# Kernel tuning notes

Hardware: AMD Instinct MI355X
Metric: run time of the kernel (lower is better)

## Reference

```python
import jax, jax.numpy as jnp
import numpy as np

N_ATOMS = 100000
IN_F = 512
HID = 512
OUT_F = 256
N_SPECIES = 64
EMB_DIM = 16
N_ROUTED = 6
N_SHARED = 2
TOPK = 2


def setup_inputs() -> dict:
    key = jax.random.key(0)
    ks = jax.random.split(key, 12)
    s = 0.02
    return {
        "features": jax.random.normal(ks[0], (N_ATOMS, IN_F), dtype=jnp.float32),
        "species_idx": jax.random.randint(ks[1], (N_ATOMS,), 0, N_SPECIES),
        "emb": jax.random.normal(ks[2], (N_SPECIES, EMB_DIM), dtype=jnp.float32),
        "W_router": jax.random.normal(ks[3], (N_ROUTED, EMB_DIM), dtype=jnp.float32) * s,
        "rW1": jax.random.normal(ks[4], (N_ROUTED, HID, IN_F), dtype=jnp.float32) * s,
        "rb1": jax.random.normal(ks[5], (N_ROUTED, HID), dtype=jnp.float32) * s,
        "rW2": jax.random.normal(ks[6], (N_ROUTED, OUT_F, HID), dtype=jnp.float32) * s,
        "rb2": jax.random.normal(ks[7], (N_ROUTED, OUT_F), dtype=jnp.float32) * s,
        "sW1": jax.random.normal(ks[8], (N_SHARED, HID, IN_F), dtype=jnp.float32) * s,
        "sb1": jax.random.normal(ks[9], (N_SHARED, HID), dtype=jnp.float32) * s,
        "sW2": jax.random.normal(ks[10], (N_SHARED, OUT_F, HID), dtype=jnp.float32) * s,
        "sb2": jax.random.normal(ks[11], (N_SHARED, OUT_F), dtype=jnp.float32) * s,
    }


def _expert_mlp(x, W1, b1, W2, b2):
    # x: [n, d]; W1: [E, h, d]; W2: [E, o, h] -> [n, E, o]
    h = jax.nn.silu(jnp.einsum("nd,ehd->neh", x, W1) + b1)
    return jnp.einsum("neh,eoh->neo", h, W2) + b2


def reference(features, species_idx, emb, W_router, rW1, rb1, rW2, rb2, sW1, sb1, sW2, sb2):
    # Router: u = SiLU(Embedding(z)); scores = softmax(W_e u)
    u = jax.nn.silu(emb[species_idx])                    # [n, M]
    scores = jax.nn.softmax(u @ W_router.T, axis=-1)     # [n, I]
    topk_scores, topk_idx = jax.lax.top_k(scores, TOPK)
    n = scores.shape[0]
    routing_weights = jnp.zeros_like(scores).at[
        jnp.arange(n)[:, None], topk_idx
    ].set(topk_scores)                                   # sparse gates [n, I]

    routed = _expert_mlp(features, rW1, rb1, rW2, rb2)   # [n, I, o]
    out = jnp.einsum("ne,neo->no", routing_weights, routed)

    shared = _expert_mlp(features, sW1, sb1, sW2, sb2)   # [n, S, o]
    return out + shared.sum(axis=1)
```

## Files before the change

kernel.cpp:

```cpp
#include <hip/hip_runtime.h>
#include <hip/hip_bf16.h>


typedef __attribute__((ext_vector_type(8))) short short8;
typedef __attribute__((ext_vector_type(4))) float f32x4;

#define IN_F 512
#define HID  512
#define OUT_F 256
#define TILE 64
#define CH   8192

#define WAIT_LGKM0 asm volatile("s_waitcnt lgkmcnt(0)" ::: "memory")
#define WAIT_VM2   asm volatile("s_waitcnt vmcnt(2)"   ::: "memory")
#define WAIT_VM0   asm volatile("s_waitcnt vmcnt(0)"   ::: "memory")

__device__ inline unsigned short f2bf(float f) {
    __hip_bfloat16 h = __float2bfloat16(f);
    return *reinterpret_cast<unsigned short*>(&h);
}

__device__ __forceinline__ void dma16(const unsigned short* g, unsigned short* l) {
    __builtin_amdgcn_global_load_lds(
        (const __attribute__((address_space(1))) unsigned int*)(unsigned long long)(const void*)g,
        (__attribute__((address_space(3))) unsigned int*)(unsigned int)(unsigned long long)(void*)l,
        16, 0, 0);
}

__device__ __forceinline__ void stage_chunk(const unsigned short* g,
                                            unsigned short* l, int w, int lane) {
    dma16(g + w * 1024 +       lane * 8, l + w * 1024);
    dma16(g + w * 1024 + 512 + lane * 8, l + w * 1024 + 512);
}

__global__ void k_cvt_w1(const float* __restrict__ rW1, const float* __restrict__ sW1,
                         unsigned short* __restrict__ dst) {
    int i = blockIdx.x * 256 + threadIdx.x;
    int low3 = i & 7;
    int sw   = (i >> 3) & 3;
    int row  = (i >> 5) & 255;
    int kq   = (i >> 13) & 15;
    int j    = (i >> 17) & 1;
    int ex   = i >> 18;
    int col  = ((sw ^ ((row >> 1) & 3)) << 3) + low3;
    int hrow = j * 256 + row;
    int kcol = kq * 32 + col;
    float v = (ex < 6) ? rW1[((size_t)ex * 512 + hrow) * 512 + kcol]
                       : sW1[((size_t)(ex - 6) * 512 + hrow) * 512 + kcol];
    dst[i] = f2bf(v);
}

__global__ void k_cvt_w2(const float* __restrict__ rW2, const float* __restrict__ sW2,
                         unsigned short* __restrict__ dst) {
    int i = blockIdx.x * 256 + threadIdx.x;
    int low3 = i & 7;
    int sw   = (i >> 3) & 3;
    int row  = (i >> 5) & 255;
    int kq   = (i >> 13) & 7;
    int j    = (i >> 16) & 1;
    int ex   = i >> 17;
    int col  = ((sw ^ ((row >> 1) & 3)) << 3) + low3;
    int kcol = j * 256 + kq * 32 + col;
    float v = (ex < 6) ? rW2[((size_t)ex * 256 + row) * 512 + kcol]
                       : sW2[((size_t)(ex - 6) * 256 + row) * 512 + kcol];
    dst[i] = f2bf(v);
}

__global__ void k_fill(int* __restrict__ counts, int* __restrict__ cursors,
                       int* __restrict__ idxl, int* __restrict__ tile_pair,
                       int CAP, int TMAX) {
    int i = blockIdx.x * 256 + threadIdx.x;
    if (i < 16) { counts[i] = 0; cursors[i] = 0; }
    if (i < TMAX) tile_pair[i] = -1;
    if (i < CAP) idxl[i] = -1;
}

__global__ void k_router(const int* __restrict__ species, const float* __restrict__ emb,
                         const float* __restrict__ Wr,
                         int* __restrict__ pid, float* __restrict__ gA, float* __restrict__ gB,
                         int* __restrict__ counts, int N) {
    __shared__ int lcnt[16];
    int tid = threadIdx.x;
    if (tid < 16) lcnt[tid] = 0;
    __syncthreads();
    int i = blockIdx.x * 256 + tid;
    if (i < N) {
        int z = species[i];
        float u[16];
#pragma unroll
        for (int k = 0; k < 16; ++k) {
            float v = emb[z * 16 + k];
            u[k] = v / (1.f + __expf(-v));
        }
        float s[6];
        float mx = -1e30f;
#pragma unroll
        for (int e = 0; e < 6; ++e) {
            float a = 0.f;
#pragma unroll
            for (int k = 0; k < 16; ++k) a += u[k] * Wr[e * 16 + k];
            s[e] = a;
            mx = fmaxf(mx, a);
        }
        float sum = 0.f;
#pragma unroll
        for (int e = 0; e < 6; ++e) { s[e] = __expf(s[e] - mx); sum += s[e]; }
        float inv = 1.f / sum;
        int i0 = 0;
#pragma unroll
        for (int e = 1; e < 6; ++e) if (s[e] > s[i0]) i0 = e;
        int i1 = (i0 == 0) ? 1 : 0;
#pragma unroll
        for (int e = 0; e < 6; ++e) if (e != i0 && s[e] > s[i1]) i1 = e;
        float g0 = s[i0] * inv, g1 = s[i1] * inv;
        int a = min(i0, i1), b = max(i0, i1);
        const int PB[5] = {0, 5, 9, 12, 14};
        int p = PB[a] + (b - a - 1);
        pid[i] = p;
        gA[i] = (a == i0) ? g0 : g1;
        gB[i] = (a == i0) ? g1 : g0;
        atomicAdd(&lcnt[p], 1);
    }
    __syncthreads();
    if (tid < 15 && lcnt[tid] > 0) atomicAdd(&counts[tid], lcnt[tid]);
}

__global__ void k_scan(const int* __restrict__ counts, int* __restrict__ offs,
                       int* __restrict__ tile_pair, int TMAX) {
    __shared__ int so[16];
    if (threadIdx.x == 0) {
        int acc = 0;
        for (int p = 0; p < 15; ++p) { so[p] = acc; acc += (counts[p] + 63) & ~63; }
        so[15] = acc;
        for (int p = 0; p < 16; ++p) offs[p] = so[p];
    }
    __syncthreads();
    for (int t = threadIdx.x; t < TMAX; t += blockDim.x) {
        int t64 = t * 64;
        if (t64 < so[15]) {
            int p = 0;
            while (!(t64 >= so[p] && t64 < so[p + 1])) ++p;
            tile_pair[t] = p;
        }
    }
}

__global__ void k_scatter(const int* __restrict__ pid, const float* __restrict__ gA,
                          const float* __restrict__ gB, const int* __restrict__ offs,
                          int* __restrict__ cursors, int* __restrict__ idxl,
                          float* __restrict__ gAl, float* __restrict__ gBl, int N) {
    __shared__ int lcnt[16], lbase[16];
    int tid = threadIdx.x;
    if (tid < 16) lcnt[tid] = 0;
    __syncthreads();
    int i = blockIdx.x * 256 + tid;
    int p = -1, rank = 0;
    if (i < N) { p = pid[i]; rank = atomicAdd(&lcnt[p], 1); }
    __syncthreads();
    if (tid < 15 && lcnt[tid] > 0) lbase[tid] = atomicAdd(&cursors[tid], lcnt[tid]);
    __syncthreads();
    if (i < N) {
        int slot = offs[p] + lbase[p] + rank;
        idxl[slot] = i; gAl[slot] = gA[i]; gBl[slot] = gB[i];
    }
}

__global__ __launch_bounds__(512, 2) void k_moe(
    const float* __restrict__ X,
    const unsigned short* __restrict__ W1pk,
    const unsigned short* __restrict__ W2pk,
    const int* __restrict__ idxl, const float* __restrict__ gAl,
    const float* __restrict__ gBl, const int* __restrict__ tile_pair,
    const float* __restrict__ rb1, const float* __restrict__ rb2,
    const float* __restrict__ sb1, const float* __restrict__ sb2,
    float* __restrict__ Y)
{
    int t;
    {
        const int nwg = (int)gridDim.x;
        const int q = nwg >> 3, r = nwg & 7;
        const int xcd = (int)blockIdx.x & 7;
        const int idx = (int)blockIdx.x >> 3;
        t = (xcd < r ? xcd * (q + 1) : r * (q + 1) + (xcd - r) * q) + idx;
    }
    const int p = tile_pair[t];
    if (p < 0) return;
    int ea = 0, eb = 1;
    {
        int pp = p;
#pragma unroll
        for (int a = 0; a < 5; ++a) {
            int span = 5 - a;
            if (pp < span) { ea = a; eb = a + 1 + pp; break; }
            pp -= span;
        }
    }

    __shared__ __align__(16) unsigned short xs[TILE][520];
    __shared__ __align__(16) unsigned short hs[TILE][264];
    __shared__ __align__(16) unsigned short wlds[3][CH];
    __shared__ float gsA[TILE], gsB[TILE];
    __shared__ int idxs[TILE];

    const int tid = threadIdx.x;
    if (tid < TILE) {
        int slot = t * TILE + tid;
        int gi = idxl[slot];
        idxs[tid] = gi;
        gsA[tid] = (gi >= 0) ? gAl[slot] : 0.f;
        gsB[tid] = (gi >= 0) ? gBl[slot] : 0.f;
    }
    __syncthreads();

    for (int i = tid; i < TILE * 128; i += 512) {
        int r = i >> 7, c4 = i & 127;
        int gi = idxs[r]; if (gi < 0) gi = 0;
        f32x4 v = __builtin_nontemporal_load(
            reinterpret_cast<const f32x4*>(X + (size_t)gi * IN_F) + c4);
        ushort4 pk;
        pk.x = f2bf(v.x); pk.y = f2bf(v.y); pk.z = f2bf(v.z); pk.w = f2bf(v.w);
        *reinterpret_cast<ushort4*>(&xs[r][c4 * 4]) = pk;
    }
    WAIT_VM0;

    const int w    = tid >> 6;
    const int lane = tid & 63;
    const int mw   = w >> 2;
    const int nw   = w & 3;
    const int quad = lane >> 4;
    const int l16  = lane & 15;
    const int swz  = ((quad ^ ((l16 >> 1) & 3)) << 3);
    const int wrow = (nw * 64 + l16) * 32;

    f32x4 outacc[2][4] = {};

    for (int ei = 0; ei < 4; ++ei) {
        const int ex = (ei == 0) ? ea : (ei == 1) ? eb : (ei + 4);
        const float* b1 = (ex < 6) ? rb1 + ex * HID   : sb1 + (ex - 6) * HID;
        const float* b2 = (ex < 6) ? rb2 + ex * OUT_F : sb2 + (ex - 6) * OUT_F;

        float gr[8];
#pragma unroll
        for (int mt = 0; mt < 2; ++mt)
#pragma unroll
            for (int r = 0; r < 4; ++r) {
                int row = mw * 32 + mt * 16 + quad * 4 + r;
                gr[mt * 4 + r] = (ei == 0) ? gsA[row] : (ei == 1) ? gsB[row] : 1.f;
            }

        for (int j = 0; j < 2; ++j) {
            const unsigned short* w1c = W1pk + ((size_t)ex * 2 + j) * (16 * CH);
            const unsigned short* w2c = W2pk + ((size_t)ex * 2 + j) * (8 * CH);

            stage_chunk(w1c,      wlds[0], w, lane);
            stage_chunk(w1c + CH, wlds[1], w, lane);

            f32x4 acc[2][4] = {};

#pragma unroll
            for (int c = 0; c < 16; ++c) {
                WAIT_LGKM0;
                WAIT_VM2;
                __builtin_amdgcn_s_barrier();
                if (c + 2 < 16)
                    stage_chunk(w1c + (c + 2) * CH, wlds[(c + 2) % 3], w, lane);
                else
                    stage_chunk(w2c + (c + 2 - 16) * CH, wlds[(c + 2) % 3], w, lane);
                const unsigned short* cur = wlds[c % 3];
                short8 b[4], a[2];
#pragma unroll
                for (int nt = 0; nt < 4; ++nt)
                    b[nt] = *reinterpret_cast<const short8*>(cur + wrow + nt * 512 + swz);
#pragma unroll
                for (int mt = 0; mt < 2; ++mt)
                    a[mt] = *reinterpret_cast<const short8*>(
                        &xs[mw * 32 + mt * 16 + l16][c * 32 + quad * 8]);
#pragma unroll
                for (int mt = 0; mt < 2; ++mt)
#pragma unroll
                    for (int nt = 0; nt < 4; ++nt)
                        acc[mt][nt] = __builtin_amdgcn_mfma_f32_16x16x32_bf16(
                            a[mt], b[nt], acc[mt][nt], 0, 0, 0);
            }

#pragma unroll
            for (int mt = 0; mt < 2; ++mt)
#pragma unroll
                for (int nt = 0; nt < 4; ++nt) {
                    int hcol = nw * 64 + nt * 16 + l16;
                    float bb = b1[j * 256 + hcol];
#pragma unroll
                    for (int r = 0; r < 4; ++r) {
                        int row = mw * 32 + mt * 16 + quad * 4 + r;
                        float v = acc[mt][nt][r] + bb;
                        float h = v / (1.f + __expf(-v));
                        hs[row][hcol] = f2bf(h * gr[mt * 4 + r]);
                    }
                }

#pragma unroll
            for (int c = 16; c < 24; ++c) {
                WAIT_LGKM0;
                if (c < 23) { WAIT_VM2; } else { WAIT_VM0; }
                __builtin_amdgcn_s_barrier();
                if (c + 2 < 24)
                    stage_chunk(w2c + (c + 2 - 16) * CH, wlds[(c + 2) % 3], w, lane);
                const unsigned short* cur = wlds[c % 3];
                short8 b[4], a[2];
#pragma unroll
                for (int nt = 0; nt < 4; ++nt)
                    b[nt] = *reinterpret_cast<const short8*>(cur + wrow + nt * 512 + swz);
#pragma unroll
                for (int mt = 0; mt < 2; ++mt)
                    a[mt] = *reinterpret_cast<const short8*>(
                        &hs[mw * 32 + mt * 16 + l16][(c - 16) * 32 + quad * 8]);
#pragma unroll
                for (int mt = 0; mt < 2; ++mt)
#pragma unroll
                    for (int nt = 0; nt < 4; ++nt)
                        outacc[mt][nt] = __builtin_amdgcn_mfma_f32_16x16x32_bf16(
                            a[mt], b[nt], outacc[mt][nt], 0, 0, 0);
            }
        }

#pragma unroll
        for (int mt = 0; mt < 2; ++mt)
#pragma unroll
            for (int nt = 0; nt < 4; ++nt) {
                float bb = b2[nw * 64 + nt * 16 + l16];
#pragma unroll
                for (int r = 0; r < 4; ++r)
                    outacc[mt][nt][r] += gr[mt * 4 + r] * bb;
            }
    }

#pragma unroll
    for (int mt = 0; mt < 2; ++mt)
#pragma unroll
        for (int nt = 0; nt < 4; ++nt)
#pragma unroll
            for (int r = 0; r < 4; ++r) {
                int row = mw * 32 + mt * 16 + quad * 4 + r;
                int gi = idxs[row];
                if (gi >= 0)
                    __builtin_nontemporal_store(outacc[mt][nt][r],
                        Y + (size_t)gi * OUT_F + nw * 64 + nt * 16 + l16);
            }
}

extern "C" void kernel_launch(void* const* d_in, const int* in_sizes, int n_in,
                              void* d_out, int out_size, void* d_ws, size_t ws_size,
                              hipStream_t stream) {
    const float* X       = (const float*)d_in[0];
    const int*   species = (const int*)d_in[1];
    const float* emb     = (const float*)d_in[2];
    const float* Wr      = (const float*)d_in[3];
    const float* rW1     = (const float*)d_in[4];
    const float* rb1     = (const float*)d_in[5];
    const float* rW2     = (const float*)d_in[6];
    const float* rb2     = (const float*)d_in[7];
    const float* sW1     = (const float*)d_in[8];
    const float* sb1     = (const float*)d_in[9];
    const float* sW2     = (const float*)d_in[10];
    const float* sb2     = (const float*)d_in[11];
    float* Y = (float*)d_out;
    const int N = in_sizes[1];

    const int TMAX = (N + 15 * 64 + 63) / 64;
    const int CAP  = TMAX * 64;

    size_t o = 0;
    auto take = [&](size_t bytes) { size_t r = o; o += (bytes + 255) & ~(size_t)255; return r; };
    char* ws = (char*)d_ws;
    unsigned short* w1bf   = (unsigned short*)(ws + take((size_t)8 * HID * IN_F * 2));
    unsigned short* w2bf   = (unsigned short*)(ws + take((size_t)8 * OUT_F * HID * 2));
    int*   pid      = (int*)  (ws + take((size_t)N * 4));
    float* gA       = (float*)(ws + take((size_t)N * 4));
    float* gB       = (float*)(ws + take((size_t)N * 4));
    int*   counts   = (int*)  (ws + take(64));
    int*   cursors  = (int*)  (ws + take(64));
    int*   offs     = (int*)  (ws + take(64));
    int*   idxl     = (int*)  (ws + take((size_t)CAP * 4));
    float* gAl      = (float*)(ws + take((size_t)CAP * 4));
    float* gBl      = (float*)(ws + take((size_t)CAP * 4));
    int*   tile_pair= (int*)  (ws + take((size_t)TMAX * 4));

    k_cvt_w1<<<(8 * HID * IN_F) / 256, 256, 0, stream>>>(rW1, sW1, w1bf);
    k_cvt_w2<<<(8 * OUT_F * HID) / 256, 256, 0, stream>>>(rW2, sW2, w2bf);
    k_fill<<<(CAP + 255) / 256, 256, 0, stream>>>(counts, cursors, idxl, tile_pair, CAP, TMAX);
    k_router<<<(N + 255) / 256, 256, 0, stream>>>(species, emb, Wr, pid, gA, gB, counts, N);
    k_scan<<<1, 256, 0, stream>>>(counts, offs, tile_pair, TMAX);
    k_scatter<<<(N + 255) / 256, 256, 0, stream>>>(pid, gA, gB, offs, cursors, idxl, gAl, gBl, N);
    k_moe<<<TMAX, 512, 0, stream>>>(X, w1bf, w2bf, idxl, gAl, gBl, tile_pair,
                                    rb1, rb2, sb1, sb2, Y);
}
```

Baseline: 839.9 us.

## Add 128-row tile MoE kernel with pre-gathered bf16 activations and fused prep

Adds a pre-pass that gathers routed activations into a contiguous bf16 buffer, then a new MoE kernel using 128-row tiles that DMA both weights and activations into LDS with a triple-buffered pipeline. The hidden activations are kept in swizzled LDS and the gate is folded into the hidden values before the second GEMM. Weight conversion and workspace fill are fused into a single prep kernel. Larger tiles raise weight reuse per row, at the cost of more padding per expert pair and an extra gather pass. The old 64-row kernel is kept as a fallback when the workspace is too small.

After: 1.172 ms. +39.5%, slower.

```diff
diff --git a/kernel.cpp b/kernel.cpp
--- a/kernel.cpp
+++ b/kernel.cpp
@@ -8,10 +8,9 @@
 #define IN_F 512
 #define HID  512
 #define OUT_F 256
-#define TILE 64
-#define CH   8192
 
 #define WAIT_LGKM0 asm volatile("s_waitcnt lgkmcnt(0)" ::: "memory")
+#define WAIT_VM3   asm volatile("s_waitcnt vmcnt(3)"   ::: "memory")
 #define WAIT_VM2   asm volatile("s_waitcnt vmcnt(2)"   ::: "memory")
 #define WAIT_VM0   asm volatile("s_waitcnt vmcnt(0)"   ::: "memory")
 
@@ -27,49 +26,45 @@
         16, 0, 0);
 }
 
-__device__ __forceinline__ void stage_chunk(const unsigned short* g,
-                                            unsigned short* l, int w, int lane) {
-    dma16(g + w * 1024 +       lane * 8, l + w * 1024);
-    dma16(g + w * 1024 + 512 + lane * 8, l + w * 1024 + 512);
-}
-
-__global__ void k_cvt_w1(const float* __restrict__ rW1, const float* __restrict__ sW1,
-                         unsigned short* __restrict__ dst) {
+__global__ void k_prep(const float* __restrict__ rW1, const float* __restrict__ sW1,
+                       const float* __restrict__ rW2, const float* __restrict__ sW2,
+                       unsigned short* __restrict__ w1bf, unsigned short* __restrict__ w2bf,
+                       int* __restrict__ counts, int* __restrict__ cursors,
+                       int* __restrict__ idxl, int* __restrict__ tile_pair,
+                       int CAP, int TMAX, int mode) {
     int i = blockIdx.x * 256 + threadIdx.x;
-    int low3 = i & 7;
-    int sw   = (i >> 3) & 3;
-    int row  = (i >> 5) & 255;
-    int kq   = (i >> 13) & 15;
-    int j    = (i >> 17) & 1;
-    int ex   = i >> 18;
-    int col  = ((sw ^ ((row >> 1) & 3)) << 3) + low3;
-    int hrow = j * 256 + row;
-    int kcol = kq * 32 + col;
-    float v = (ex < 6) ? rW1[((size_t)ex * 512 + hrow) * 512 + kcol]
-                       : sW1[((size_t)(ex - 6) * 512 + hrow) * 512 + kcol];
-    dst[i] = f2bf(v);
-}
-
-__global__ void k_cvt_w2(const float* __restrict__ rW2, const float* __restrict__ sW2,
-                         unsigned short* __restrict__ dst) {
-    int i = blockIdx.x * 256 + threadIdx.x;
-    int low3 = i & 7;
-    int sw   = (i >> 3) & 3;
-    int row  = (i >> 5) & 255;
-    int kq   = (i >> 13) & 7;
-    int j    = (i >> 16) & 1;
-    int ex   = i >> 17;
-    int col  = ((sw ^ ((row >> 1) & 3)) << 3) + low3;
-    int kcol = j * 256 + kq * 32 + col;
-    float v = (ex < 6) ? rW2[((size_t)ex * 256 + row) * 512 + kcol]
-                       : sW2[((size_t)(ex - 6) * 256 + row) * 512 + kcol];
-    dst[i] = f2bf(v);
-}
-
-__global__ void k_fill(int* __restrict__ counts, int* __restrict__ cursors,
-                       int* __restrict__ idxl, int* __restrict__ tile_pair,
-                       int CAP, int TMAX) {
-    int i = blockIdx.x * 256 + threadIdx.x;
+    if (i < 8 * 512 * 512) {
+        float v;
+        if (mode == 0) {
+            int e = i >> 18, off = i & ((1 << 18) - 1);
+            v = (e < 6) ? rW1[(size_t)e * 262144 + off]
+                        : sW1[(size_t)(e - 6) * 262144 + off];
+        } else {
+            int low3 = i & 7, sw = (i >> 3) & 3, row = (i >> 5) & 255;
+            int kq = (i >> 13) & 15, j = (i >> 17) & 1, ex = i >> 18;
+            int col = ((sw ^ ((row >> 1) & 3)) << 3) + low3;
+            int hrow = j * 256 + row, kcol = kq * 32 + col;
+            v = (ex < 6) ? rW1[((size_t)ex * 512 + hrow) * 512 + kcol]
+                         : sW1[((size_t)(ex - 6) * 512 + hrow) * 512 + kcol];
+        }
+        w1bf[i] = f2bf(v);
+    }
+    if (i < 8 * 256 * 512) {
+        float v;
+        if (mode == 0) {
+            int e = i >> 17, off = i & ((1 << 17) - 1);
+            v = (e < 6) ? rW2[(size_t)e * 131072 + off]
+                        : sW2[(size_t)(e - 6) * 131072 + off];
+        } else {
+            int low3 = i & 7, sw = (i >> 3) & 3, row = (i >> 5) & 255;
+            int kq = (i >> 13) & 7, j = (i >> 16) & 1, ex = i >> 17;
+            int col = ((sw ^ ((row >> 1) & 3)) << 3) + low3;
+            int kcol = j * 256 + kq * 32 + col;
+            v = (ex < 6) ? rW2[((size_t)ex * 256 + row) * 512 + kcol]
+                         : sW2[((size_t)(ex - 6) * 256 + row) * 512 + kcol];
+        }
+        w2bf[i] = f2bf(v);
+    }
     if (i < 16) { counts[i] = 0; cursors[i] = 0; }
     if (i < TMAX) tile_pair[i] = -1;
     if (i < CAP) idxl[i] = -1;
@@ -126,20 +121,20 @@
 }
 
 __global__ void k_scan(const int* __restrict__ counts, int* __restrict__ offs,
-                       int* __restrict__ tile_pair, int TMAX) {
+                       int* __restrict__ tile_pair, int TMAX, int P) {
     __shared__ int so[16];
     if (threadIdx.x == 0) {
         int acc = 0;
-        for (int p = 0; p < 15; ++p) { so[p] = acc; acc += (counts[p] + 63) & ~63; }
+        for (int p = 0; p < 15; ++p) { so[p] = acc; acc += (counts[p] + P - 1) & ~(P - 1); }
         so[15] = acc;
         for (int p = 0; p < 16; ++p) offs[p] = so[p];
     }
     __syncthreads();
     for (int t = threadIdx.x; t < TMAX; t += blockDim.x) {
-        int t64 = t * 64;
-        if (t64 < so[15]) {
+        int tP = t * P;
+        if (tP < so[15]) {
             int p = 0;
-            while (!(t64 >= so[p] && t64 < so[p + 1])) ++p;
+            while (!(tP >= so[p] && tP < so[p + 1])) ++p;
             tile_pair[t] = p;
         }
     }
@@ -165,7 +160,244 @@
     }
 }
 
-__global__ __launch_bounds__(512, 2) void k_moe(
+__global__ void k_gather(const float* __restrict__ X, const int* __restrict__ idxl,
+                         unsigned short* __restrict__ Xbf, int CAP) {
+    int i = blockIdx.x * 256 + threadIdx.x;
+    int slot = i >> 6;
+    if (slot >= CAP) return;
+    int k8 = (i & 63) * 8;
+    int gi = idxl[slot];
+    ushort4 pk0 = {0, 0, 0, 0}, pk1 = {0, 0, 0, 0};
+    if (gi >= 0) {
+        f32x4 v0 = __builtin_nontemporal_load(
+            reinterpret_cast<const f32x4*>(X + (size_t)gi * IN_F + k8));
+        f32x4 v1 = __builtin_nontemporal_load(
+            reinterpret_cast<const f32x4*>(X + (size_t)gi * IN_F + k8 + 4));
+        pk0.x = f2bf(v0.x); pk0.y = f2bf(v0.y); pk0.z = f2bf(v0.z); pk0.w = f2bf(v0.w);
+        pk1.x = f2bf(v1.x); pk1.y = f2bf(v1.y); pk1.z = f2bf(v1.z); pk1.w = f2bf(v1.w);
+    }
+    *reinterpret_cast<ushort4*>(Xbf + (size_t)slot * 512 + k8) = pk0;
+    *reinterpret_cast<ushort4*>(Xbf + (size_t)slot * 512 + k8 + 4) = pk1;
+}
+
+__global__ __launch_bounds__(512, 2) void k_moe_v2(
+    const unsigned short* __restrict__ Xbf,
+    const unsigned short* __restrict__ W1b,
+    const unsigned short* __restrict__ W2b,
+    const int* __restrict__ idxl, const float* __restrict__ gAl,
+    const float* __restrict__ gBl, const int* __restrict__ tile_pair,
+    const float* __restrict__ rb1, const float* __restrict__ rb2,
+    const float* __restrict__ sb1, const float* __restrict__ sb2,
+    float* __restrict__ Y)
+{
+    int t;
+    {
+        const int nwg = (int)gridDim.x;
+        const int q = nwg >> 3, r = nwg & 7;
+        const int xcd = (int)blockIdx.x & 7;
+        const int idx = (int)blockIdx.x >> 3;
+        t = (xcd < r ? xcd * (q + 1) : r * (q + 1) + (xcd - r) * q) + idx;
+    }
+    const int p = tile_pair[t];
+    if (p < 0) return;
+    int ea = 0, eb = 1;
+    {
+        int pp = p;
+#pragma unroll
+        for (int a = 0; a < 5; ++a) {
+            int span = 5 - a;
+            if (pp < span) { ea = a; eb = a + 1 + pp; break; }
+            pp -= span;
+        }
+    }
+
+    __shared__ __align__(16) unsigned short Wl[3][8192];
+    __shared__ __align__(16) unsigned short Xl[3][4096];
+    __shared__ __align__(16) unsigned short hsl[32768];
+    __shared__ float gsA[128], gsB[128];
+    __shared__ int idxs[128];
+
+    const int tid  = threadIdx.x;
+    const int w    = tid >> 6;
+    const int lane = tid & 63;
+    const int quad = lane >> 4;
+    const int l16  = lane & 15;
+    const int mw   = w >> 2;
+    const int nw   = w & 3;
+
+    const int kxs = (((lane & 3) ^ ((lane >> 3) & 3)) << 3);
+    const size_t wg = (size_t)(32 * w + (lane >> 2)) * 512 + kxs;
+    const size_t xg = ((size_t)t * 128 + 16 * w + (lane >> 2)) * 512 + kxs;
+
+    const int wswz = ((quad ^ ((l16 >> 1) & 3)) << 3);
+    const int wro  = (nw * 64 + l16) * 32 + wswz;
+    const int xro  = (mw * 64 + l16) * 32 + wswz;
+    const int hro  = (mw * 64 + l16) * 256;
+
+    unsigned short* const wdst = &Wl[0][0];
+    unsigned short* const xdst = &Xl[0][0];
+
+    auto stageA = [&](int s, const unsigned short* w1u, int kq) {
+        dma16(w1u + wg + kq * 32,        wdst + s * 8192 + w * 1024);
+        dma16(w1u + wg + 8192 + kq * 32, wdst + s * 8192 + w * 1024 + 512);
+        dma16(Xbf + xg + kq * 32,        xdst + s * 4096 + w * 512);
+    };
+    auto stageB = [&](int s, const unsigned short* w2u, int b) {
+        dma16(w2u + wg + b * 32,        wdst + s * 8192 + w * 1024);
+        dma16(w2u + wg + 8192 + b * 32, wdst + s * 8192 + w * 1024 + 512);
+    };
+
+    const unsigned short* w1u0 = W1b + (size_t)ea * 262144;
+
+    stageA(0, w1u0, 0);
+    stageA(1, w1u0, 1);
+
+    if (tid < 128) {
+        int slot = t * 128 + tid;
+        int gi = idxl[slot];
+        idxs[tid] = gi;
+        gsA[tid] = (gi >= 0) ? gAl[slot] : 0.f;
+        gsB[tid] = (gi >= 0) ? gBl[slot] : 0.f;
+    }
+    WAIT_LGKM0;
+    __builtin_amdgcn_s_barrier();
+
+    f32x4 outacc[4][4] = {};
+    float gr[16];
+
+    for (int p8 = 0; p8 < 8; ++p8) {
+        const int ei = p8 >> 1, j = p8 & 1;
+        const int ex = (ei == 0) ? ea : (ei == 1) ? eb : (ei + 4);
+        const unsigned short* w1u = W1b + (size_t)ex * 262144 + (size_t)j * 131072;
+        const unsigned short* w2u = W2b + (size_t)ex * 131072 + (size_t)j * 256;
+        const float* b1 = (ex < 6) ? rb1 + ex * HID   : sb1 + (ex - 6) * HID;
+        const float* b2 = (ex < 6) ? rb2 + ex * OUT_F : sb2 + (ex - 6) * OUT_F;
+        const int p8n = p8 + 1;
+        const int ein = p8n >> 1, jn = p8n & 1;
+        const int exn = (ein == 0) ? ea : (ein == 1) ? eb : (ein + 4);
+        const unsigned short* w1un = (p8 < 7)
+            ? W1b + (size_t)exn * 262144 + (size_t)jn * 131072 : w1u;
+
+        if (j == 0) {
+#pragma unroll
+            for (int mt = 0; mt < 4; ++mt)
+#pragma unroll
+                for (int r = 0; r < 4; ++r) {
+                    int row = mw * 64 + mt * 16 + quad * 4 + r;
+                    gr[mt * 4 + r] = (ei == 0) ? gsA[row] : (ei == 1) ? gsB[row] : 1.f;
+                }
+        }
+
+        f32x4 acc[4][4] = {};
+
+#pragma unroll
+        for (int c = 0; c < 16; ++c) {
+            WAIT_LGKM0;
+            if (c < 15) { WAIT_VM3; } else { WAIT_VM2; }
+            __builtin_amdgcn_s_barrier();
+            if (c <= 13)      stageA((c + 2) % 3, w1u, c + 2);
+            else if (c == 14) stageB(1, w2u, 0);
+            else              stageB(2, w2u, 1);
+            const unsigned short* wc = &Wl[c % 3][0];
+            const unsigned short* xc = &Xl[c % 3][0];
+            short8 bfr[4], afr[4];
+#pragma unroll
+            for (int nt = 0; nt < 4; ++nt)
+                bfr[nt] = *reinterpret_cast<const short8*>(wc + wro + nt * 512);
+#pragma unroll
+            for (int mt = 0; mt < 4; ++mt)
+                afr[mt] = *reinterpret_cast<const short8*>(xc + xro + mt * 512);
+            __builtin_amdgcn_s_setprio(1);
+#pragma unroll
+            for (int mt = 0; mt < 4; ++mt)
+#pragma unroll
+                for (int nt = 0; nt < 4; ++nt)
+                    acc[mt][nt] = __builtin_amdgcn_mfma_f32_16x16x32_bf16(
+                        afr[mt], bfr[nt], acc[mt][nt], 0, 0, 0);
+            __builtin_amdgcn_s_setprio(0);
+        }
+
+#pragma unroll
+        for (int mt = 0; mt < 4; ++mt)
+#pragma unroll
+            for (int nt = 0; nt < 4; ++nt) {
+                int col = nw * 64 + nt * 16 + l16;
+                float bb = b1[j * 256 + col];
+#pragma unroll
+                for (int r = 0; r < 4; ++r) {
+                    int row = mw * 64 + mt * 16 + quad * 4 + r;
+                    float v = acc[mt][nt][r] + bb;
+                    float h = v / (1.f + __expf(-v));
+                    int sl = ((col >> 3) ^ (row & 7));
+                    hsl[row * 256 + sl * 8 + (col & 7)] = f2bf(h * gr[mt * 4 + r]);
+                }
+            }
+
+#pragma unroll
+        for (int b = 0; b < 8; ++b) {
+            WAIT_LGKM0;
+            if (b < 7) { WAIT_VM2; }
+            else if (p8 < 7) { WAIT_VM3; } else { WAIT_VM0; }
+            __builtin_amdgcn_s_barrier();
+            if (b <= 5)               stageB(b % 3, w2u, b + 2);
+            else if (b == 6 && p8 < 7) stageA(0, w1un, 0);
+            else if (b == 7 && p8 < 7) stageA(1, w1un, 1);
+            const unsigned short* wc = &Wl[(b + 1) % 3][0];
+            short8 bfr[4], afr[4];
+#pragma unroll
+            for (int nt = 0; nt < 4; ++nt)
+                bfr[nt] = *reinterpret_cast<const short8*>(wc + wro + nt * 512);
+#pragma unroll
+            for (int mt = 0; mt < 4; ++mt)
+                afr[mt] = *reinterpret_cast<const short8*>(
+                    hsl + hro + mt * 4096 + ((((b * 4) + quad) ^ (l16 & 7)) << 3));
+            __builtin_amdgcn_s_setprio(1);
+#pragma unroll
+            for (int mt = 0; mt < 4; ++mt)
+#pragma unroll
+                for (int nt = 0; nt < 4; ++nt)
+                    outacc[mt][nt] = __builtin_amdgcn_mfma_f32_16x16x32_bf16(
+                        afr[mt], bfr[nt], outacc[mt][nt], 0, 0, 0);
+            __builtin_amdgcn_s_setprio(0);
+        }
+
+        if (j == 1) {
+#pragma unroll
+            for (int mt = 0; mt < 4; ++mt)
+#pragma unroll
+                for (int nt = 0; nt < 4; ++nt) {
+                    float bb = b2[nw * 64 + nt * 16 + l16];
+#pragma unroll
+                    for (int r = 0; r < 4; ++r)
+                        outacc[mt][nt][r] += gr[mt * 4 + r] * bb;
+                }
+        }
+    }
+
+#pragma unroll
+    for (int mt = 0; mt < 4; ++mt)
+#pragma unroll
+        for (int nt = 0; nt < 4; ++nt)
+#pragma unroll
+            for (int r = 0; r < 4; ++r) {
+                int row = mw * 64 + mt * 16 + quad * 4 + r;
+                int gi = idxs[row];
+                if (gi >= 0)
+                    __builtin_nontemporal_store(outacc[mt][nt][r],
+                        Y + (size_t)gi * OUT_F + nw * 64 + nt * 16 + l16);
+            }
+}
+
+#define TILE 64
+#define CH   8192
+
+__device__ __forceinline__ void stage_chunk(const unsigned short* g,
+                                            unsigned short* l, int w, int lane) {
+    dma16(g + w * 1024 +       lane * 8, l + w * 1024);
+    dma16(g + w * 1024 + 512 + lane * 8, l + w * 1024 + 512);
+}
+
+__global__ __launch_bounds__(512, 2) void k_moe_v1(
     const float* __restrict__ X,
     const unsigned short* __restrict__ W1pk,
     const unsigned short* __restrict__ W2pk,
@@ -366,14 +598,30 @@
     float* Y = (float*)d_out;
     const int N = in_sizes[1];
 
-    const int TMAX = (N + 15 * 64 + 63) / 64;
-    const int CAP  = TMAX * 64;
+    const int TMAX128 = (N + 15 * 128 + 127) / 128;
+    const int CAP128  = TMAX128 * 128;
+    const int TMAX64  = (N + 15 * 64 + 63) / 64;
+    const int CAP64   = TMAX64 * 64;
+
+    size_t fixed = 0;
+    auto sz = [&](size_t b) { fixed += (b + 255) & ~(size_t)255; };
+    sz((size_t)8 * HID * IN_F * 2); sz((size_t)8 * OUT_F * HID * 2);
+    sz((size_t)N * 4); sz((size_t)N * 4); sz((size_t)N * 4);
+    sz(64); sz(64); sz(64);
+    sz((size_t)CAP128 * 4); sz((size_t)CAP128 * 4); sz((size_t)CAP128 * 4);
+    sz((size_t)TMAX128 * 4);
+    const size_t xbf_bytes = (size_t)CAP128 * 512 * 2;
+    const bool big = (fixed + xbf_bytes + 256) <= ws_size;
+
+    const int P    = big ? 128 : 64;
+    const int TMAX = big ? TMAX128 : TMAX64;
+    const int CAP  = big ? CAP128 : CAP64;
 
     size_t o = 0;
     auto take = [&](size_t bytes) { size_t r = o; o += (bytes + 255) & ~(size_t)255; return r; };
     char* ws = (char*)d_ws;
-    unsigned short* w1bf   = (unsigned short*)(ws + take((size_t)8 * HID * IN_F * 2));
-    unsigned short* w2bf   = (unsigned short*)(ws + take((size_t)8 * OUT_F * HID * 2));
+    unsigned short* w1bf = (unsigned short*)(ws + take((size_t)8 * HID * IN_F * 2));
+    unsigned short* w2bf = (unsigned short*)(ws + take((size_t)8 * OUT_F * HID * 2));
     int*   pid      = (int*)  (ws + take((size_t)N * 4));
     float* gA       = (float*)(ws + take((size_t)N * 4));
     float* gB       = (float*)(ws + take((size_t)N * 4));
@@ -384,13 +632,20 @@
     float* gAl      = (float*)(ws + take((size_t)CAP * 4));
     float* gBl      = (float*)(ws + take((size_t)CAP * 4));
     int*   tile_pair= (int*)  (ws + take((size_t)TMAX * 4));
-
-    k_cvt_w1<<<(8 * HID * IN_F) / 256, 256, 0, stream>>>(rW1, sW1, w1bf);
-    k_cvt_w2<<<(8 * OUT_F * HID) / 256, 256, 0, stream>>>(rW2, sW2, w2bf);
-    k_fill<<<(CAP + 255) / 256, 256, 0, stream>>>(counts, cursors, idxl, tile_pair, CAP, TMAX);
+    unsigned short* Xbf = big ? (unsigned short*)(ws + take(xbf_bytes)) : nullptr;
+
+    k_prep<<<12288, 256, 0, stream>>>(rW1, sW1, rW2, sW2, w1bf, w2bf,
+                                      counts, cursors, idxl, tile_pair,
+                                      CAP, TMAX, big ? 0 : 1);
     k_router<<<(N + 255) / 256, 256, 0, stream>>>(species, emb, Wr, pid, gA, gB, counts, N);
-    k_scan<<<1, 256, 0, stream>>>(counts, offs, tile_pair, TMAX);
+    k_scan<<<1, 256, 0, stream>>>(counts, offs, tile_pair, TMAX, P);
     k_scatter<<<(N + 255) / 256, 256, 0, stream>>>(pid, gA, gB, offs, cursors, idxl, gAl, gBl, N);
-    k_moe<<<TMAX, 512, 0, stream>>>(X, w1bf, w2bf, idxl, gAl, gBl, tile_pair,
-                                    rb1, rb2, sb1, sb2, Y);
-}
+    if (big) {
+        k_gather<<<CAP / 4, 256, 0, stream>>>(X, idxl, Xbf, CAP);
+        k_moe_v2<<<TMAX, 512, 0, stream>>>(Xbf, w1bf, w2bf, idxl, gAl, gBl, tile_pair,
+                                           rb1, rb2, sb1, sb2, Y);
+    } else {
+        k_moe_v1<<<TMAX, 512, 0, stream>>>(X, w1bf, w2bf, idxl, gAl, gBl, tile_pair,
+                                           rb1, rb2, sb1, sb2, Y);
+    }
+}
```

## Restructure MoE weight pipeline to four-buffer double-chunk staging with cross-expert prefetch

Applied to the files above, without the earlier changes.

Fuses the weight conversion and workspace fill kernels into a single prep kernel, removing two launches. The MoE kernel now uses a 4-slot LDS ring that consumes two K-chunks per barrier, which halves the barrier count. It prefetches the next expert's first W1 chunks during the W2 phase and raises MFMA issue priority with setprio. X and H tiles are stored in a swizzled k-chunked LDS layout, and the gate and index shared arrays are replaced with direct global reads. The costs are higher LDS usage and a full vmcnt(0) wait at every step.

Result: slower. 870.0 us (+3.6%).

```diff
diff --git a/kernel.cpp b/kernel.cpp
--- a/kernel.cpp
+++ b/kernel.cpp
@@ -12,7 +12,7 @@
 #define CH   8192
 
 #define WAIT_LGKM0 asm volatile("s_waitcnt lgkmcnt(0)" ::: "memory")
-#define WAIT_VM2   asm volatile("s_waitcnt vmcnt(2)"   ::: "memory")
+#define WAIT_VM4   asm volatile("s_waitcnt vmcnt(4)"   ::: "memory")
 #define WAIT_VM0   asm volatile("s_waitcnt vmcnt(0)"   ::: "memory")
 
 __device__ inline unsigned short f2bf(float f) {
@@ -27,49 +27,31 @@
         16, 0, 0);
 }
 
-__device__ __forceinline__ void stage_chunk(const unsigned short* g,
-                                            unsigned short* l, int w, int lane) {
-    dma16(g + w * 1024 +       lane * 8, l + w * 1024);
-    dma16(g + w * 1024 + 512 + lane * 8, l + w * 1024 + 512);
-}
-
-__global__ void k_cvt_w1(const float* __restrict__ rW1, const float* __restrict__ sW1,
-                         unsigned short* __restrict__ dst) {
-    int i = blockIdx.x * 256 + threadIdx.x;
-    int low3 = i & 7;
-    int sw   = (i >> 3) & 3;
-    int row  = (i >> 5) & 255;
-    int kq   = (i >> 13) & 15;
-    int j    = (i >> 17) & 1;
-    int ex   = i >> 18;
-    int col  = ((sw ^ ((row >> 1) & 3)) << 3) + low3;
-    int hrow = j * 256 + row;
-    int kcol = kq * 32 + col;
-    float v = (ex < 6) ? rW1[((size_t)ex * 512 + hrow) * 512 + kcol]
-                       : sW1[((size_t)(ex - 6) * 512 + hrow) * 512 + kcol];
-    dst[i] = f2bf(v);
-}
-
-__global__ void k_cvt_w2(const float* __restrict__ rW2, const float* __restrict__ sW2,
-                         unsigned short* __restrict__ dst) {
-    int i = blockIdx.x * 256 + threadIdx.x;
-    int low3 = i & 7;
-    int sw   = (i >> 3) & 3;
-    int row  = (i >> 5) & 255;
-    int kq   = (i >> 13) & 7;
-    int j    = (i >> 16) & 1;
-    int ex   = i >> 17;
-    int col  = ((sw ^ ((row >> 1) & 3)) << 3) + low3;
-    int kcol = j * 256 + kq * 32 + col;
-    float v = (ex < 6) ? rW2[((size_t)ex * 256 + row) * 512 + kcol]
-                       : sW2[((size_t)(ex - 6) * 256 + row) * 512 + kcol];
-    dst[i] = f2bf(v);
-}
-
-__global__ void k_fill(int* __restrict__ counts, int* __restrict__ cursors,
+__global__ void k_prep(const float* __restrict__ rW1, const float* __restrict__ sW1,
+                       const float* __restrict__ rW2, const float* __restrict__ sW2,
+                       unsigned short* __restrict__ w1bf, unsigned short* __restrict__ w2bf,
+                       int* __restrict__ counts, int* __restrict__ cursors,
                        int* __restrict__ idxl, int* __restrict__ tile_pair,
                        int CAP, int TMAX) {
     int i = blockIdx.x * 256 + threadIdx.x;
+    if (i < 8 * 512 * 512) {
+        int low3 = i & 7, sw = (i >> 3) & 3, row = (i >> 5) & 255;
+        int kq = (i >> 13) & 15, j = (i >> 17) & 1, ex = i >> 18;
+        int col = ((sw ^ ((row >> 1) & 3)) << 3) + low3;
+        int hrow = j * 256 + row, kcol = kq * 32 + col;
+        float v = (ex < 6) ? rW1[((size_t)ex * 512 + hrow) * 512 + kcol]
+                           : sW1[((size_t)(ex - 6) * 512 + hrow) * 512 + kcol];
+        w1bf[i] = f2bf(v);
+    }
+    if (i < 8 * 256 * 512) {
+        int low3 = i & 7, sw = (i >> 3) & 3, row = (i >> 5) & 255;
+        int kq = (i >> 13) & 7, j = (i >> 16) & 1, ex = i >> 17;
+        int col = ((sw ^ ((row >> 1) & 3)) << 3) + low3;
+        int kcol = j * 256 + kq * 32 + col;
+        float v = (ex < 6) ? rW2[((size_t)ex * 256 + row) * 512 + kcol]
+                           : sW2[((size_t)(ex - 6) * 256 + row) * 512 + kcol];
+        w2bf[i] = f2bf(v);
+    }
     if (i < 16) { counts[i] = 0; cursors[i] = 0; }
     if (i < TMAX) tile_pair[i] = -1;
     if (i < CAP) idxl[i] = -1;
@@ -196,156 +178,195 @@
         }
     }
 
-    __shared__ __align__(16) unsigned short xs[TILE][520];
-    __shared__ __align__(16) unsigned short hs[TILE][264];
-    __shared__ __align__(16) unsigned short wlds[3][CH];
-    __shared__ float gsA[TILE], gsB[TILE];
-    __shared__ int idxs[TILE];
-
-    const int tid = threadIdx.x;
-    if (tid < TILE) {
-        int slot = t * TILE + tid;
-        int gi = idxl[slot];
-        idxs[tid] = gi;
-        gsA[tid] = (gi >= 0) ? gAl[slot] : 0.f;
-        gsB[tid] = (gi >= 0) ? gBl[slot] : 0.f;
-    }
-    __syncthreads();
+    __shared__ __align__(16) unsigned short xs[16][64][32];
+    __shared__ __align__(16) unsigned short hl[8][64][32];
+    __shared__ __align__(16) unsigned short wl[4][CH];
+
+    const int tid  = threadIdx.x;
+    const int w    = tid >> 6;
+    const int lane = tid & 63;
+    const int quad = lane >> 4;
+    const int l16  = lane & 15;
+    const int mw   = w >> 2;
+    const int nw   = w & 3;
 
     for (int i = tid; i < TILE * 128; i += 512) {
-        int r = i >> 7, c4 = i & 127;
-        int gi = idxs[r]; if (gi < 0) gi = 0;
+        int row = i >> 7, c4 = i & 127;
+        int gi = idxl[t * TILE + row]; if (gi < 0) gi = 0;
         f32x4 v = __builtin_nontemporal_load(
             reinterpret_cast<const f32x4*>(X + (size_t)gi * IN_F) + c4);
         ushort4 pk;
         pk.x = f2bf(v.x); pk.y = f2bf(v.y); pk.z = f2bf(v.z); pk.w = f2bf(v.w);
-        *reinterpret_cast<ushort4*>(&xs[r][c4 * 4]) = pk;
+        int kq   = c4 >> 3;
+        int slot = ((c4 >> 1) & 3) ^ ((row >> 1) & 3);
+        *reinterpret_cast<ushort4*>(&xs[kq][row][slot * 8 + (c4 & 1) * 4]) = pk;
     }
     WAIT_VM0;
 
-    const int w    = tid >> 6;
-    const int lane = tid & 63;
-    const int mw   = w >> 2;
-    const int nw   = w & 3;
-    const int quad = lane >> 4;
-    const int l16  = lane & 15;
+    auto stW = [&](const unsigned short* src, int buf) {
+        dma16(src + w * 1024 +       lane * 8, &wl[buf][w * 1024]);
+        dma16(src + w * 1024 + 512 + lane * 8, &wl[buf][w * 1024 + 512]);
+    };
+
     const int swz  = ((quad ^ ((l16 >> 1) & 3)) << 3);
-    const int wrow = (nw * 64 + l16) * 32;
+    const int wro  = (nw * 64 + l16) * 32 + swz;
+    const int xrow = mw * 32 + l16;
+
+    {
+        const unsigned short* w1c0 = W1pk + (size_t)(ea * 2) * (16 * CH);
+        stW(w1c0,          0); stW(w1c0 + CH,     1);
+        stW(w1c0 + 2 * CH, 2); stW(w1c0 + 3 * CH, 3);
+    }
+    WAIT_LGKM0;
+    WAIT_VM4;
+    __builtin_amdgcn_s_barrier();
 
     f32x4 outacc[2][4] = {};
-
-    for (int ei = 0; ei < 4; ++ei) {
+    float gr[8];
+
+    for (int p8 = 0; p8 < 8; ++p8) {
+        const int ei = p8 >> 1, j = p8 & 1;
         const int ex = (ei == 0) ? ea : (ei == 1) ? eb : (ei + 4);
+        const unsigned short* w1c = W1pk + (size_t)(ex * 2 + j) * (16 * CH);
+        const unsigned short* w2c = W2pk + (size_t)(ex * 2 + j) * (8 * CH);
         const float* b1 = (ex < 6) ? rb1 + ex * HID   : sb1 + (ex - 6) * HID;
         const float* b2 = (ex < 6) ? rb2 + ex * OUT_F : sb2 + (ex - 6) * OUT_F;
-
-        float gr[8];
-#pragma unroll
-        for (int mt = 0; mt < 2; ++mt)
-#pragma unroll
-            for (int r = 0; r < 4; ++r) {
-                int row = mw * 32 + mt * 16 + quad * 4 + r;
-                gr[mt * 4 + r] = (ei == 0) ? gsA[row] : (ei == 1) ? gsB[row] : 1.f;
-            }
-
-        for (int j = 0; j < 2; ++j) {
-            const unsigned short* w1c = W1pk + ((size_t)ex * 2 + j) * (16 * CH);
-            const unsigned short* w2c = W2pk + ((size_t)ex * 2 + j) * (8 * CH);
-
-            stage_chunk(w1c,      wlds[0], w, lane);
-            stage_chunk(w1c + CH, wlds[1], w, lane);
-
-            f32x4 acc[2][4] = {};
-
-#pragma unroll
-            for (int c = 0; c < 16; ++c) {
-                WAIT_LGKM0;
-                WAIT_VM2;
-                __builtin_amdgcn_s_barrier();
-                if (c + 2 < 16)
-                    stage_chunk(w1c + (c + 2) * CH, wlds[(c + 2) % 3], w, lane);
-                else
-                    stage_chunk(w2c + (c + 2 - 16) * CH, wlds[(c + 2) % 3], w, lane);
-                const unsigned short* cur = wlds[c % 3];
-                short8 b[4], a[2];
+        const int ein = (p8 + 1) >> 1, jn = (p8 + 1) & 1;
+        const int exn = (ein == 0) ? ea : (ein == 1) ? eb : (ein + 4);
+        const unsigned short* w1cN = W1pk + (size_t)((p8 < 7 ? exn : ex) * 2 + jn) * (16 * CH);
+
+        if (j == 0) {
+            const float* gp = (ei == 0) ? gAl : (ei == 1) ? gBl : nullptr;
+#pragma unroll
+            for (int mt = 0; mt < 2; ++mt)
+#pragma unroll
+                for (int r = 0; r < 4; ++r) {
+                    int row = mw * 32 + mt * 16 + quad * 4 + r;
+                    gr[mt * 4 + r] = gp ? gp[t * TILE + row] : 1.f;
+                }
+        }
+
+        f32x4 acc[2][4] = {};
+
+#pragma unroll
+        for (int d = 0; d < 8; ++d) {
+            short8 bfr[2][4], afr[2][2];
+#pragma unroll
+            for (int kk = 0; kk < 2; ++kk) {
+                const unsigned short* wc = &wl[(2 * d + kk) & 3][0];
 #pragma unroll
                 for (int nt = 0; nt < 4; ++nt)
-                    b[nt] = *reinterpret_cast<const short8*>(cur + wrow + nt * 512 + swz);
+                    bfr[kk][nt] = *reinterpret_cast<const short8*>(wc + wro + nt * 512);
 #pragma unroll
                 for (int mt = 0; mt < 2; ++mt)
-                    a[mt] = *reinterpret_cast<const short8*>(
-                        &xs[mw * 32 + mt * 16 + l16][c * 32 + quad * 8]);
+                    afr[kk][mt] = *reinterpret_cast<const short8*>(
+                        &xs[2 * d + kk][xrow + mt * 16][swz]);
+            }
+            __builtin_amdgcn_s_setprio(1);
+#pragma unroll
+            for (int kk = 0; kk < 2; ++kk)
 #pragma unroll
                 for (int mt = 0; mt < 2; ++mt)
 #pragma unroll
                     for (int nt = 0; nt < 4; ++nt)
                         acc[mt][nt] = __builtin_amdgcn_mfma_f32_16x16x32_bf16(
-                            a[mt], b[nt], acc[mt][nt], 0, 0, 0);
-            }
-
-#pragma unroll
-            for (int mt = 0; mt < 2; ++mt)
-#pragma unroll
-                for (int nt = 0; nt < 4; ++nt) {
-                    int hcol = nw * 64 + nt * 16 + l16;
-                    float bb = b1[j * 256 + hcol];
-#pragma unroll
-                    for (int r = 0; r < 4; ++r) {
-                        int row = mw * 32 + mt * 16 + quad * 4 + r;
-                        float v = acc[mt][nt][r] + bb;
-                        float h = v / (1.f + __expf(-v));
-                        hs[row][hcol] = f2bf(h * gr[mt * 4 + r]);
-                    }
+                            afr[kk][mt], bfr[kk][nt], acc[mt][nt], 0, 0, 0);
+            __builtin_amdgcn_s_setprio(0);
+            WAIT_LGKM0;
+            WAIT_VM0;
+            __builtin_amdgcn_s_barrier();
+            const int s0 = 2 * d + 4;
+            if (s0 < 16) {
+                stW(w1c + (size_t)s0 * CH, s0 & 3);
+                stW(w1c + (size_t)(s0 + 1) * CH, (s0 + 1) & 3);
+            } else {
+                stW(w2c + (size_t)(s0 - 16) * CH, s0 & 3);
+                stW(w2c + (size_t)(s0 - 15) * CH, (s0 + 1) & 3);
+            }
+        }
+
+#pragma unroll
+        for (int mt = 0; mt < 2; ++mt)
+#pragma unroll
+            for (int nt = 0; nt < 4; ++nt) {
+                int hcol = nw * 64 + nt * 16 + l16;
+                float bb = b1[j * 256 + hcol];
+                int kq = hcol >> 5, ic = hcol & 31;
+#pragma unroll
+                for (int r = 0; r < 4; ++r) {
+                    int row = mw * 32 + mt * 16 + quad * 4 + r;
+                    float v = acc[mt][nt][r] + bb;
+                    float h = v / (1.f + __expf(-v));
+                    int sl = (ic >> 3) ^ ((row >> 1) & 3);
+                    hl[kq][row][sl * 8 + (ic & 7)] = f2bf(h * gr[mt * 4 + r]);
                 }
-
-#pragma unroll
-            for (int c = 16; c < 24; ++c) {
-                WAIT_LGKM0;
-                if (c < 23) { WAIT_VM2; } else { WAIT_VM0; }
-                __builtin_amdgcn_s_barrier();
-                if (c + 2 < 24)
-                    stage_chunk(w2c + (c + 2 - 16) * CH, wlds[(c + 2) % 3], w, lane);
-                const unsigned short* cur = wlds[c % 3];
-                short8 b[4], a[2];
+            }
+        WAIT_LGKM0;
+        __builtin_amdgcn_s_barrier();
+
+#pragma unroll
+        for (int d = 0; d < 4; ++d) {
+            short8 bfr[2][4], afr[2][2];
+#pragma unroll
+            for (int kk = 0; kk < 2; ++kk) {
+                const unsigned short* wc = &wl[(2 * d + kk) & 3][0];
 #pragma unroll
                 for (int nt = 0; nt < 4; ++nt)
-                    b[nt] = *reinterpret_cast<const short8*>(cur + wrow + nt * 512 + swz);
+                    bfr[kk][nt] = *reinterpret_cast<const short8*>(wc + wro + nt * 512);
 #pragma unroll
                 for (int mt = 0; mt < 2; ++mt)
-                    a[mt] = *reinterpret_cast<const short8*>(
-                        &hs[mw * 32 + mt * 16 + l16][(c - 16) * 32 + quad * 8]);
+                    afr[kk][mt] = *reinterpret_cast<const short8*>(
+                        &hl[2 * d + kk][xrow + mt * 16][swz]);
+            }
+            __builtin_amdgcn_s_setprio(1);
+#pragma unroll
+            for (int kk = 0; kk < 2; ++kk)
 #pragma unroll
                 for (int mt = 0; mt < 2; ++mt)
 #pragma unroll
                     for (int nt = 0; nt < 4; ++nt)
                         outacc[mt][nt] = __builtin_amdgcn_mfma_f32_16x16x32_bf16(
-                            a[mt], b[nt], outacc[mt][nt], 0, 0, 0);
-            }
-        }
-
-#pragma unroll
-        for (int mt = 0; mt < 2; ++mt)
-#pragma unroll
-            for (int nt = 0; nt < 4; ++nt) {
-                float bb = b2[nw * 64 + nt * 16 + l16];
-#pragma unroll
-                for (int r = 0; r < 4; ++r)
-                    outacc[mt][nt][r] += gr[mt * 4 + r] * bb;
-            }
+                            afr[kk][mt], bfr[kk][nt], outacc[mt][nt], 0, 0, 0);
+            __builtin_amdgcn_s_setprio(0);
+            WAIT_LGKM0;
+            WAIT_VM0;
+            __builtin_amdgcn_s_barrier();
+            const int s0 = 20 + 2 * d;
+            if (s0 < 24) {
+                stW(w2c + (size_t)(s0 - 16) * CH, s0 & 3);
+                stW(w2c + (size_t)(s0 - 15) * CH, (s0 + 1) & 3);
+            } else if (p8 < 7) {
+                stW(w1cN + (size_t)(s0 - 24) * CH, s0 & 3);
+                stW(w1cN + (size_t)(s0 - 23) * CH, (s0 + 1) & 3);
+            }
+        }
+
+        if (j == 1) {
+#pragma unroll
+            for (int mt = 0; mt < 2; ++mt)
+#pragma unroll
+                for (int nt = 0; nt < 4; ++nt) {
+                    float bb = b2[nw * 64 + nt * 16 + l16];
+#pragma unroll
+                    for (int r = 0; r < 4; ++r)
+                        outacc[mt][nt][r] += gr[mt * 4 + r] * bb;
+                }
+        }
     }
 
 #pragma unroll
     for (int mt = 0; mt < 2; ++mt)
 #pragma unroll
-        for (int nt = 0; nt < 4; ++nt)
-#pragma unroll
-            for (int r = 0; r < 4; ++r) {
-                int row = mw * 32 + mt * 16 + quad * 4 + r;
-                int gi = idxs[row];
-                if (gi >= 0)
+        for (int r = 0; r < 4; ++r) {
+            int row = mw * 32 + mt * 16 + quad * 4 + r;
+            int gi = idxl[t * TILE + row];
+            if (gi >= 0) {
+#pragma unroll
+                for (int nt = 0; nt < 4; ++nt)
                     __builtin_nontemporal_store(outacc[mt][nt][r],
                         Y + (size_t)gi * OUT_F + nw * 64 + nt * 16 + l16);
             }
+        }
 }
 
 extern "C" void kernel_launch(void* const* d_in, const int* in_sizes, int n_in,
@@ -372,8 +393,8 @@
     size_t o = 0;
     auto take = [&](size_t bytes) { size_t r = o; o += (bytes + 255) & ~(size_t)255; return r; };
     char* ws = (char*)d_ws;
-    unsigned short* w1bf   = (unsigned short*)(ws + take((size_t)8 * HID * IN_F * 2));
-    unsigned short* w2bf   = (unsigned short*)(ws + take((size_t)8 * OUT_F * HID * 2));
+    unsigned short* w1bf = (unsigned short*)(ws + take((size_t)8 * HID * IN_F * 2));
+    unsigned short* w2bf = (unsigned short*)(ws + take((size_t)8 * OUT_F * HID * 2));
     int*   pid      = (int*)  (ws + take((size_t)N * 4));
     float* gA       = (float*)(ws + take((size_t)N * 4));
     float* gB       = (float*)(ws + take((size_t)N * 4));
@@ -385,9 +406,8 @@
     float* gBl      = (float*)(ws + take((size_t)CAP * 4));
     int*   tile_pair= (int*)  (ws + take((size_t)TMAX * 4));
 
-    k_cvt_w1<<<(8 * HID * IN_F) / 256, 256, 0, stream>>>(rW1, sW1, w1bf);
-    k_cvt_w2<<<(8 * OUT_F * HID) / 256, 256, 0, stream>>>(rW2, sW2, w2bf);
-    k_fill<<<(CAP + 255) / 256, 256, 0, stream>>>(counts, cursors, idxl, tile_pair, CAP, TMAX);
+    k_prep<<<8192, 256, 0, stream>>>(rW1, sW1, rW2, sW2, w1bf, w2bf,
+                                     counts, cursors, idxl, tile_pair, CAP, TMAX);
     k_router<<<(N + 255) / 256, 256, 0, stream>>>(species, emb, Wr, pid, gA, gB, counts, N);
     k_scan<<<1, 256, 0, stream>>>(counts, offs, tile_pair, TMAX);
     k_scatter<<<(N + 255) / 256, 256, 0, stream>>>(pid, gA, gB, offs, cursors, idxl, gAl, gBl, N);
```
